# Performance work log

Measured on AMD Instinct MI355X. Metric: run time of the kernel, lower is better.

The kernel has to match this reference:

```python
import jax, jax.numpy as jnp
import numpy as np

# Keras GRUCell (reset_after=True, default in TF2) step
# Keras LSTMCell step (gate order i, f, c, o)
# Keras RNN masking semantics: at masked steps, states are frozen and the
# step output is the previous output (equivalent to freezing every layer's h).

def _gru_step(a, h, W, U, bi, br):
    gx = a @ W + bi          # [B, 3H] input projection
    gh = h @ U + br          # [B, 3H] recurrent projection (reset_after)
    xz, xr, xh = jnp.split(gx, 3, axis=-1)
    rz, rr, rh = jnp.split(gh, 3, axis=-1)
    z = jax.nn.sigmoid(xz + rz)
    r = jax.nn.sigmoid(xr + rr)
    hh = jnp.tanh(xh + r * rh)
    return z * h + (1.0 - z) * hh


def _lstm_step(a, h, c, W, U, b):
    g = a @ W + h @ U + b    # [B, 4H]
    gi, gf, gc, go = jnp.split(g, 4, axis=-1)
    i = jax.nn.sigmoid(gi)
    f = jax.nn.sigmoid(gf)
    cn = f * c + i * jnp.tanh(gc)
    hn = jax.nn.sigmoid(go) * jnp.tanh(cn)
    return hn, cn


def run_gru_stack(x, mask, layers):
    # x: [B,T,D], mask: [B,T] bool; layers: list of (W,U,bi,br)
    B = x.shape[0]
    H = layers[0][1].shape[0]
    xT = jnp.swapaxes(x, 0, 1)      # [T,B,D]
    mT = jnp.swapaxes(mask, 0, 1)   # [T,B]

    def step(hs, inp):
        xt, mt = inp
        a = xt
        new = []
        for (W, U, bi, br), h in zip(layers, hs):
            hn = _gru_step(a, h, W, U, bi, br)
            hn = jnp.where(mt[:, None], hn, h)  # freeze state under mask
            new.append(hn)
            a = hn
        return tuple(new), a

    h0 = tuple(jnp.zeros((B, H), x.dtype) for _ in layers)
    _, ys = jax.lax.scan(step, h0, (xT, mT))
    return jnp.swapaxes(ys, 0, 1)   # [B,T,H]


def run_lstm_stack(x, mask, layers):
    # layers: list of (W,U,b)
    B = x.shape[0]
    H = layers[0][1].shape[0]
    xT = jnp.swapaxes(x, 0, 1)
    mT = jnp.swapaxes(mask, 0, 1)

    def step(state, inp):
        xt, mt = inp
        a = xt
        new = []
        for (W, U, b), (h, c) in zip(layers, state):
            hn, cn = _lstm_step(a, h, c, W, U, b)
            hn = jnp.where(mt[:, None], hn, h)
            cn = jnp.where(mt[:, None], cn, c)
            new.append((hn, cn))
            a = hn
        return tuple(new), a

    s0 = tuple((jnp.zeros((B, H), x.dtype), jnp.zeros((B, H), x.dtype)) for _ in layers)
    _, ys = jax.lax.scan(step, s0, (xT, mT))
    return jnp.swapaxes(ys, 0, 1)


def _forward(x, lengths, g_W0, g_U0, g_bi0, g_br0, g_W1, g_U1, g_bi1, g_br1,
             l_W0, l_U0, l_b0, l_W1, l_U1, l_b1, out_W, out_b):
    T = x.shape[1]
    mask = jnp.arange(T)[None, :] < lengths[:, None]          # [B,T]
    o1 = run_gru_stack(x, mask, [(g_W0, g_U0, g_bi0, g_br0),
                                 (g_W1, g_U1, g_bi1, g_br1)])  # [B,T,H]
    o2 = run_lstm_stack(x, mask, [(l_W0, l_U0, l_b0),
                                  (l_W1, l_U1, l_b1)])          # [B,T,H]
    c = jnp.concatenate([o1, o2], axis=-1)                      # [B,T,2H]
    return c @ out_W + out_b                                    # [B,T,1]


def setup_inputs() -> dict:
    key = jax.random.key(0)
    ks = jax.random.split(key, 16)
    B, T, D, H = 64, 512, 96, 256
    glorot = lambda k, shp: (jax.random.normal(k, shp, dtype=jnp.float32)
                             / np.sqrt(shp[0]).astype(np.float32))
    inp = {
        "x": jax.random.normal(ks[0], (B, T, D), dtype=jnp.float32),
        "lengths": jax.random.randint(ks[1], (B,), 1, T + 1),
        # GRU stack (reset_after: separate input/recurrent biases)
        "g_W0": glorot(ks[2], (D, 3 * H)),
        "g_U0": glorot(ks[3], (H, 3 * H)),
        "g_bi0": jnp.zeros((3 * H,), jnp.float32),
        "g_br0": jnp.zeros((3 * H,), jnp.float32),
        "g_W1": glorot(ks[4], (H, 3 * H)),
        "g_U1": glorot(ks[5], (H, 3 * H)),
        "g_bi1": jnp.zeros((3 * H,), jnp.float32),
        "g_br1": jnp.zeros((3 * H,), jnp.float32),
        # LSTM stack
        "l_W0": glorot(ks[6], (D, 4 * H)),
        "l_U0": glorot(ks[7], (H, 4 * H)),
        "l_b0": jnp.zeros((4 * H,), jnp.float32),
        "l_W1": glorot(ks[8], (H, 4 * H)),
        "l_U1": glorot(ks[9], (H, 4 * H)),
        "l_b1": jnp.zeros((4 * H,), jnp.float32),
        # Dense head on concat [.., 2H] -> 1
        "out_W": glorot(ks[10], (2 * H, 1)),
        "out_b": jnp.zeros((1,), jnp.float32),
    }
    return inp


def reference(x, lengths, g_W0, g_U0, g_bi0, g_br0, g_W1, g_U1, g_bi1, g_br1,
              l_W0, l_U0, l_b0, l_W1, l_U1, l_b1, out_W, out_b):
    return _forward(x, lengths, g_W0, g_U0, g_bi0, g_br0, g_W1, g_U1, g_bi1,
                    g_br1, l_W0, l_U0, l_b0, l_W1, l_U1, l_b1, out_W, out_b)
```

## Files before the change

kernel.cpp:

```cpp
#include <hip/hip_runtime.h>
#include <hip/hip_fp16.h>

constexpr int Tt = 512, Dd = 96, Hh = 256;
constexpr int NS0 = 16;
constexpr int NSP = 8;
typedef unsigned long long u64;

constexpr size_t OFF_P0  = (size_t)4 << 20;
constexpr size_t OFF_P1  = (size_t)12 << 20;
constexpr size_t OFF_FLG = (size_t)20 << 20;
constexpr size_t OFF_W16 = ((size_t)20 << 20) + ((size_t)64 << 10);
constexpr size_t oGW0 = 0;
constexpr size_t oGU0 = oGW0 + (size_t)48 * 768;
constexpr size_t oGW1 = oGU0 + (size_t)128 * 768;
constexpr size_t oGU1 = oGW1 + (size_t)128 * 768;
constexpr size_t oLW0 = oGU1 + (size_t)128 * 768;
constexpr size_t oLU0 = oLW0 + (size_t)48 * 1024;
constexpr size_t oLW1 = oLU0 + (size_t)128 * 1024;
constexpr size_t oLU1 = oLW1 + (size_t)128 * 1024;

__device__ __forceinline__ float sigf(float v) { return 1.0f / (1.0f + __expf(-v)); }
__device__ __forceinline__ u64 agld(const u64* p) {
    return __hip_atomic_load(p, __ATOMIC_RELAXED, __HIP_MEMORY_SCOPE_AGENT);
}
__device__ __forceinline__ int agldi(const int* p) {
    return __hip_atomic_load(p, __ATOMIC_ACQUIRE, __HIP_MEMORY_SCOPE_AGENT);
}
__device__ __forceinline__ void agst(u64* p, u64 v) {
    __hip_atomic_store(p, v, __ATOMIC_RELAXED, __HIP_MEMORY_SCOPE_AGENT);
}

__device__ __forceinline__ float dot2f(unsigned w, unsigned a, float acc) {
#if __has_builtin(__builtin_amdgcn_fdot2)
    typedef _Float16 h2v __attribute__((ext_vector_type(2)));
    h2v wh, ah;
    __builtin_memcpy(&wh, &w, 4);
    __builtin_memcpy(&ah, &a, 4);
    return __builtin_amdgcn_fdot2(wh, ah, acc, false);
#else
    const float2 wf = __half22float2(*(const __half2*)&w);
    const float2 af = __half22float2(*(const __half2*)&a);
    acc = fmaf(wf.x, af.x, acc);
    return fmaf(wf.y, af.y, acc);
#endif
}

__device__ __forceinline__ int hidx(int k, int r) {
    return (k >> 1) * 8 + r * 2 + (k & 1);
}

template<int G>
__device__ __forceinline__ void load4h(uint4* wv, const uint4* __restrict__ M4,
                                       int ldm, int kpb) {
    const int base = (kpb >> 2) * ldm;
    #pragma unroll
    for (int g = 0; g < G; ++g)
        wv[g] = M4[base + g * 256];
}
template<int G>
__device__ __forceinline__ void fma4h(const uint4* wv, const uint4* __restrict__ A4,
                                      int kpb, float4* acc) {
    const uint4 a0 = A4[kpb + 0];
    const uint4 a1 = A4[kpb + 1];
    const uint4 a2 = A4[kpb + 2];
    const uint4 a3 = A4[kpb + 3];
    #pragma unroll
    for (int g = 0; g < G; ++g) {
        const uint4 w = wv[g];
        acc[g].x = dot2f(w.x, a0.x, acc[g].x);
        acc[g].y = dot2f(w.x, a0.y, acc[g].y);
        acc[g].z = dot2f(w.x, a0.z, acc[g].z);
        acc[g].w = dot2f(w.x, a0.w, acc[g].w);
        acc[g].x = dot2f(w.y, a1.x, acc[g].x);
        acc[g].y = dot2f(w.y, a1.y, acc[g].y);
        acc[g].z = dot2f(w.y, a1.z, acc[g].z);
        acc[g].w = dot2f(w.y, a1.w, acc[g].w);
        acc[g].x = dot2f(w.z, a2.x, acc[g].x);
        acc[g].y = dot2f(w.z, a2.y, acc[g].y);
        acc[g].z = dot2f(w.z, a2.z, acc[g].z);
        acc[g].w = dot2f(w.z, a2.w, acc[g].w);
        acc[g].x = dot2f(w.w, a3.x, acc[g].x);
        acc[g].y = dot2f(w.w, a3.y, acc[g].y);
        acc[g].z = dot2f(w.w, a3.z, acc[g].z);
        acc[g].w = dot2f(w.w, a3.w, acc[g].w);
    }
}
template<int G>
__device__ __forceinline__ void gemmP(const uint4* __restrict__ M4, int ldm,
                                      const uint4* __restrict__ A4,
                                      int kp0, int kp1, float4* acc) {
    const int n4 = (kp1 - kp0) >> 2;
    uint4 wv0[G], wv1[G];
    if (n4 <= 0) return;
    load4h<G>(wv0, M4, ldm, kp0);
    int c2 = 0;
    for (; c2 + 2 <= n4; c2 += 2) {
        load4h<G>(wv1, M4, ldm, kp0 + (c2 + 1) * 4);
        fma4h<G>(wv0, A4, kp0 + c2 * 4, acc);
        if (c2 + 2 < n4) load4h<G>(wv0, M4, ldm, kp0 + (c2 + 2) * 4);
        fma4h<G>(wv1, A4, kp0 + (c2 + 1) * 4, acc);
    }
    if (c2 < n4) fma4h<G>(wv0, A4, kp0 + c2 * 4, acc);
}

__global__ void cvt_pair(const float* __restrict__ src, unsigned* __restrict__ dst,
                         int n, int ld) {
    const int i = blockIdx.x * 256 + threadIdx.x;
    if (i >= n) return;
    const int kp = i / ld, col = i - kp * ld;
    const __half2 h = __floats2half2_rn(src[(2 * kp) * ld + col],
                                        src[(2 * kp + 1) * ld + col]);
    dst[((size_t)((kp >> 2) * ld + col) << 2) + (kp & 3)] = *(const unsigned*)&h;
}

__global__ void __launch_bounds__(1024, 4)
rnn_persist(const float* __restrict__ x, const int* __restrict__ lengths,
            const float* __restrict__ gbi0, const float* __restrict__ gbr0,
            const float* __restrict__ gbi1, const float* __restrict__ gbr1,
            const float* __restrict__ lb0, const float* __restrict__ lb1,
            const float* __restrict__ outW, const float* __restrict__ outb,
            float* __restrict__ out, char* __restrict__ wsb)
{
    const int tid = threadIdx.x;
    const int c   = tid & 255;
    const int grp = tid >> 8;
    const int bx  = blockIdx.x;
    const int role  = bx & 3;
    const int chain = (bx >> 2) & 1;
    const int rg    = bx >> 3;
    const int rowbase = rg * 4;

    const int GA  = chain ? 4 : 3;
    const int GAH = GA * Hh;

    u64* h0ring = (u64*)wsb + (size_t)(chain * 16 + rg) * (NS0 * 1024);
    u64* p0ring = (u64*)(wsb + OFF_P0) + (size_t)(chain * 16 + rg) * (NSP * 4096);
    u64* p1ring = (u64*)(wsb + OFF_P1) + (size_t)(chain * 16 + rg) * (NSP * 4096);
    int* flags = (int*)(wsb + OFF_FLG);
    int* flg_r0 = flags + ((chain * 16 + rg) * 4 + 1) * 32;
    int* flg_p1 = flags + ((chain * 16 + rg) * 4 + 2) * 32;
    int* flg_r1 = flags + ((chain * 16 + rg) * 4 + 3) * 32;

    const unsigned* W16 = (const unsigned*)(wsb + OFF_W16);
    size_t woff;
    if (chain == 0) woff = (role == 0) ? oGW0 : (role == 1) ? oGU0 : (role == 2) ? oGW1 : oGU1;
    else            woff = (role == 0) ? oLW0 : (role == 1) ? oLU0 : (role == 2) ? oLW1 : oLU1;
    const uint4* M4 = (const uint4*)(W16 + woff) + c;

    const int KR  = (role == 0) ? Dd : Hh;
    const int KP2 = KR >> 3;
    const int kp0 = grp * KP2, kp1 = kp0 + KP2;

    __shared__ __align__(16) unsigned sAh[128 * 4];
    __shared__ float sG[2 * 4096];
    __shared__ float sP[4096];
    __shared__ float sRed[16];
    __half* sAhh = (__half*)sAh;
    const uint4* A4 = (const uint4*)sAh;

    const int NP  = 4 * GAH;
    const int npt = NP >> 10;
    float biasv[4];
    int sgidx[4];
    if (role == 0 || role == 2) {
        const float* bsrc = (chain == 0) ? (role == 0 ? gbi0 : gbi1)
                                         : (role == 0 ? lb0 : lb1);
        #pragma unroll
        for (int i = 0; i < 4; ++i) {
            if (i < npt) {
                const int e = tid + i * 1024;
                const int r = e / GAH, rem = e - r * GAH;
                biasv[i] = bsrc[rem];
                sgidx[i] = r * 1024 + rem;
            } else { biasv[i] = 0; sgidx[i] = 0; }
        }
    }
    const int rA = grp;
    const int lenA = lengths[rowbase + rA];
    float brz = 0, brr = 0, brh = 0, ow = 0;
    if (chain == 0 && (role == 1 || role == 3)) {
        const float* br = (role == 1) ? gbr0 : gbr1;
        brz = br[c]; brr = br[Hh + c]; brh = br[2 * Hh + c];
    }
    if (role == 3) ow = outW[chain * Hh + c];
    const float outb0 = outb[0];
    float creg = 0.0f;
    float hprev = 0.0f;

    for (int i = tid; i < 512; i += 1024) sAh[i] = 0;
    __syncthreads();

    for (int t = 0; t < Tt; ++t) {
        if (role == 0) {
            if (t >= NSP) {
                if (tid == 0)
                    while (agldi(flg_r0) < t - NSP + 1) __builtin_amdgcn_s_sleep(1);
                __syncthreads();
            }
            if (tid < 4 * Dd) {
                const int r = tid / Dd, k = tid - r * Dd;
                const float v = x[((size_t)(rowbase + r) * Tt + t) * Dd + k];
                sAhh[hidx(k, r)] = __float2half(v);
            }
            __syncthreads();
        } else if (role == 2) {
            const u64* p0 = h0ring + (size_t)(t & (NS0 - 1)) * 1024 + rA * 256 + c;
            const unsigned want = (unsigned)(t + 1);
            u64 v0;
            do { v0 = agld(p0); } while ((unsigned)v0 != want);
            sAhh[hidx(c, rA)] = __float2half(__uint_as_float((unsigned)(v0 >> 32)));
            __syncthreads();
            if (tid == 0)
                __hip_atomic_exchange(flg_p1, t + 1, __ATOMIC_RELEASE,
                                      __HIP_MEMORY_SCOPE_AGENT);
        } else {
            const u64* slot = ((role == 1) ? p0ring : p1ring)
                              + (size_t)(t & (NSP - 1)) * 4096;
            const unsigned want = (unsigned)(t + 1);
            unsigned dm = 0;
            const unsigned full = (1u << npt) - 1u;
            while (dm != full) {
                for (int i = 0; i < npt; ++i) {
                    if (!(dm & (1u << i))) {
                        const u64 v = agld(slot + tid + i * 1024);
                        if ((unsigned)v == want) {
                            sP[tid + i * 1024] = __uint_as_float((unsigned)(v >> 32));
                            dm |= 1u << i;
                        }
                    }
                }
            }
            __syncthreads();
            if (tid == 0)
                __hip_atomic_exchange((role == 1) ? flg_r0 : flg_r1, t + 1,
                                      __ATOMIC_RELEASE, __HIP_MEMORY_SCOPE_AGENT);
        }

        if (chain == 0) {
            float4 acc[3] = {{0,0,0,0},{0,0,0,0},{0,0,0,0}};
            gemmP<3>(M4, GAH, A4, kp0, kp1, acc);
            if (grp < 2) {
                #pragma unroll
                for (int g = 0; g < 3; ++g) {
                    sG[grp * 4096 + 0 + g * 256 + c]    = acc[g].x;
                    sG[grp * 4096 + 1024 + g * 256 + c] = acc[g].y;
                    sG[grp * 4096 + 2048 + g * 256 + c] = acc[g].z;
                    sG[grp * 4096 + 3072 + g * 256 + c] = acc[g].w;
                }
            }
            __syncthreads();
            if (grp >= 2) {
                const int b = (grp - 2) * 4096;
                #pragma unroll
                for (int g = 0; g < 3; ++g) {
                    sG[b + 0 + g * 256 + c]    += acc[g].x;
                    sG[b + 1024 + g * 256 + c] += acc[g].y;
                    sG[b + 2048 + g * 256 + c] += acc[g].z;
                    sG[b + 3072 + g * 256 + c] += acc[g].w;
                }
            }
        } else {
            float4 acc[4] = {{0,0,0,0},{0,0,0,0},{0,0,0,0},{0,0,0,0}};
            gemmP<4>(M4, GAH, A4, kp0, kp1, acc);
            if (grp < 2) {
                #pragma unroll
                for (int g = 0; g < 4; ++g) {
                    sG[grp * 4096 + 0 + g * 256 + c]    = acc[g].x;
                    sG[grp * 4096 + 1024 + g * 256 + c] = acc[g].y;
                    sG[grp * 4096 + 2048 + g * 256 + c] = acc[g].z;
                    sG[grp * 4096 + 3072 + g * 256 + c] = acc[g].w;
                }
            }
            __syncthreads();
            if (grp >= 2) {
                const int b = (grp - 2) * 4096;
                #pragma unroll
                for (int g = 0; g < 4; ++g) {
                    sG[b + 0 + g * 256 + c]    += acc[g].x;
                    sG[b + 1024 + g * 256 + c] += acc[g].y;
                    sG[b + 2048 + g * 256 + c] += acc[g].z;
                    sG[b + 3072 + g * 256 + c] += acc[g].w;
                }
            }
        }
        __syncthreads();

        if (role == 0 || role == 2) {
            if (role == 2 && t >= NSP) {
                if (tid == 0)
                    while (agldi(flg_r1) < t - NSP + 1) __builtin_amdgcn_s_sleep(1);
                __syncthreads();
            }
            u64* ring = (role == 0) ? p0ring : p1ring;
            u64* slot = ring + (size_t)(t & (NSP - 1)) * 4096;
            for (int i = 0; i < npt; ++i) {
                const float v = sG[sgidx[i]] + sG[4096 + sgidx[i]] + biasv[i];
                agst(slot + tid + i * 1024,
                     ((u64)__float_as_uint(v) << 32) | (unsigned)(t + 1));
            }
        } else {
            if (role == 1 && t >= NS0) {
                if (tid == 0)
                    while (agldi(flg_p1) < t - NS0 + 1) __builtin_amdgcn_s_sleep(1);
                __syncthreads();
            }
            const int r = rA;
            const float hold = hprev;
            float hn;
            if (chain == 0) {
                const float Pz = sP[r * GAH + c];
                const float Pr = sP[r * GAH + Hh + c];
                const float Ph = sP[r * GAH + 2 * Hh + c];
                const float Qz = sG[r * 1024 + c]       + sG[4096 + r * 1024 + c];
                const float Qr = sG[r * 1024 + 256 + c] + sG[4096 + r * 1024 + 256 + c];
                const float Qh = sG[r * 1024 + 512 + c] + sG[4096 + r * 1024 + 512 + c];
                const float z  = sigf(Pz + Qz + brz);
                const float rr = sigf(Pr + Qr + brr);
                const float hh = tanhf(Ph + rr * (Qh + brh));
                hn = z * hold + (1.0f - z) * hh;
                if (t >= lenA) hn = hold;
            } else {
                const float gi = sP[r * GAH + c]          + sG[r * 1024 + c]       + sG[4096 + r * 1024 + c];
                const float gf = sP[r * GAH + Hh + c]     + sG[r * 1024 + 256 + c] + sG[4096 + r * 1024 + 256 + c];
                const float gc = sP[r * GAH + 2 * Hh + c] + sG[r * 1024 + 512 + c] + sG[4096 + r * 1024 + 512 + c];
                const float go = sP[r * GAH + 3 * Hh + c] + sG[r * 1024 + 768 + c] + sG[4096 + r * 1024 + 768 + c];
                float cn = sigf(gf) * creg + sigf(gi) * tanhf(gc);
                hn = sigf(go) * tanhf(cn);
                if (t >= lenA) { hn = hold; cn = creg; }
                creg = cn;
            }
            hprev = hn;
            sAhh[hidx(c, r)] = __float2half(hn);
            if (role == 1) {
                agst(h0ring + (size_t)(t & (NS0 - 1)) * 1024 + r * 256 + c,
                     ((u64)__float_as_uint(hn) << 32) | (unsigned)(t + 1));
            } else {
                float vh = hn * ow;
                for (int o = 32; o > 0; o >>= 1)
                    vh += __shfl_down(vh, o);
                if ((tid & 63) == 0) sRed[tid >> 6] = vh;
                __syncthreads();
                if (tid < 4) {
                    const float s = sRed[tid * 4] + sRed[tid * 4 + 1]
                                  + sRed[tid * 4 + 2] + sRed[tid * 4 + 3];
                    atomicAdd(&out[(size_t)(rowbase + tid) * Tt + t],
                              s + (chain ? outb0 : 0.0f));
                }
            }
        }
        __syncthreads();
    }
}

extern "C" void kernel_launch(void* const* d_in, const int* in_sizes, int n_in,
                              void* d_out, int out_size, void* d_ws, size_t ws_size,
                              hipStream_t stream) {
    const float* x       = (const float*)d_in[0];
    const int*   lengths = (const int*)d_in[1];
    const float* gW0  = (const float*)d_in[2];
    const float* gU0  = (const float*)d_in[3];
    const float* gbi0 = (const float*)d_in[4];
    const float* gbr0 = (const float*)d_in[5];
    const float* gW1  = (const float*)d_in[6];
    const float* gU1  = (const float*)d_in[7];
    const float* gbi1 = (const float*)d_in[8];
    const float* gbr1 = (const float*)d_in[9];
    const float* lW0  = (const float*)d_in[10];
    const float* lU0  = (const float*)d_in[11];
    const float* lb0  = (const float*)d_in[12];
    const float* lW1  = (const float*)d_in[13];
    const float* lU1  = (const float*)d_in[14];
    const float* lb1  = (const float*)d_in[15];
    const float* outW = (const float*)d_in[16];
    const float* outb = (const float*)d_in[17];
    float* out = (float*)d_out;
    char* wsb  = (char*)d_ws;

    hipMemsetAsync(d_ws, 0, OFF_FLG + (16 << 10), stream);
    hipMemsetAsync(d_out, 0, (size_t)out_size * sizeof(float), stream);

    unsigned* W16 = (unsigned*)(wsb + OFF_W16);
    struct { const float* s; size_t o; int K; int ld; } cv[8] = {
        {gW0, oGW0, 96, 768}, {gU0, oGU0, 256, 768},
        {gW1, oGW1, 256, 768}, {gU1, oGU1, 256, 768},
        {lW0, oLW0, 96, 1024}, {lU0, oLU0, 256, 1024},
        {lW1, oLW1, 256, 1024}, {lU1, oLU1, 256, 1024},
    };
    for (int i = 0; i < 8; ++i) {
        const int n = (cv[i].K / 2) * cv[i].ld;
        cvt_pair<<<(n + 255) / 256, 256, 0, stream>>>(cv[i].s, W16 + cv[i].o, n, cv[i].ld);
    }

    rnn_persist<<<dim3(128), dim3(1024), 0, stream>>>(
        x, lengths, gbi0, gbr0, gbi1, gbr1, lb0, lb1, outW, outb, out, wsb);
}
```

Baseline: 5.410 ms.

## Split RNN persistent kernel into 8 roles per chain with column-sliced weights

Restructures the persistent RNN kernel from 4 roles of 1024 threads to 8 roles of 512 threads per chain/row-group (256 blocks). Each layer's recurrent matmul is now split across two or four blocks by hidden-unit slices, and each recurrent block computes its own gate nonlinearity. Layer-1 blocks fuse the W1/U1 products instead of going through a separate projection ring. Weights are reconverted into per-slice fp16 layouts, and synchronisation now uses multiple per-slice flags plus a new h1 ring. The aim is to shorten the per-timestep critical path by spreading the recurrent GEMV over more CUs, at the cost of more cross-block polling traffic and sync points.

```diff
diff --git a/kernel.cpp b/kernel.cpp
--- a/kernel.cpp
+++ b/kernel.cpp
@@ -3,21 +3,22 @@
 
 constexpr int Tt = 512, Dd = 96, Hh = 256;
 constexpr int NS0 = 16;
+constexpr int NS1 = 16;
 constexpr int NSP = 8;
 typedef unsigned long long u64;
 
+constexpr size_t OFF_H0  = 0;
 constexpr size_t OFF_P0  = (size_t)4 << 20;
-constexpr size_t OFF_P1  = (size_t)12 << 20;
+constexpr size_t OFF_H1  = (size_t)12 << 20;
 constexpr size_t OFF_FLG = (size_t)20 << 20;
 constexpr size_t OFF_W16 = ((size_t)20 << 20) + ((size_t)64 << 10);
-constexpr size_t oGW0 = 0;
-constexpr size_t oGU0 = oGW0 + (size_t)48 * 768;
-constexpr size_t oGW1 = oGU0 + (size_t)128 * 768;
-constexpr size_t oGU1 = oGW1 + (size_t)128 * 768;
-constexpr size_t oLW0 = oGU1 + (size_t)128 * 768;
-constexpr size_t oLU0 = oLW0 + (size_t)48 * 1024;
-constexpr size_t oLW1 = oLU0 + (size_t)128 * 1024;
-constexpr size_t oLU1 = oLW1 + (size_t)128 * 1024;
+
+constexpr size_t sG_p0 = (size_t)384 * 48,  oG_p0 = 0;
+constexpr size_t sG_r0 = (size_t)384 * 128, oG_r0 = oG_p0 + 2 * sG_p0;
+constexpr size_t sG_r1 = (size_t)192 * 256, oG_r1 = oG_r0 + 2 * sG_r0;
+constexpr size_t sL_p0 = (size_t)512 * 48,  oL_p0 = oG_r1 + 4 * sG_r1;
+constexpr size_t sL_r0 = (size_t)512 * 128, oL_r0 = oL_p0 + 2 * sL_p0;
+constexpr size_t sL_r1 = (size_t)256 * 256, oL_r1 = oL_r0 + 2 * sL_r0;
 
 __device__ __forceinline__ float sigf(float v) { return 1.0f / (1.0f + __expf(-v)); }
 __device__ __forceinline__ u64 agld(const u64* p) {
@@ -28,6 +29,22 @@
 }
 __device__ __forceinline__ void agst(u64* p, u64 v) {
     __hip_atomic_store(p, v, __ATOMIC_RELAXED, __HIP_MEMORY_SCOPE_AGENT);
+}
+__device__ __forceinline__ void xrel(int* p, int v) {
+    __hip_atomic_exchange(p, v, __ATOMIC_RELEASE, __HIP_MEMORY_SCOPE_AGENT);
+}
+__device__ __forceinline__ float pollF(const u64* p, unsigned want) {
+    u64 v = agld(p);
+    while ((unsigned)v != want) v = agld(p);
+    return __uint_as_float((unsigned)(v >> 32));
+}
+__device__ __forceinline__ void waitFlags(const int* flg, int fid0, int n, int need) {
+    for (;;) {
+        int m = 0x7fffffff;
+        for (int i = 0; i < n; ++i) m = min(m, agldi(flg + (fid0 + i) * 32));
+        if (m >= need) break;
+        __builtin_amdgcn_s_sleep(1);
+    }
 }
 
 __device__ __forceinline__ float dot2f(unsigned w, unsigned a, float acc) {
@@ -49,71 +66,71 @@
     return (k >> 1) * 8 + r * 2 + (k & 1);
 }
 
-template<int G>
-__device__ __forceinline__ void load4h(uint4* wv, const uint4* __restrict__ M4,
-                                       int ldm, int kpb) {
-    const int base = (kpb >> 2) * ldm;
-    #pragma unroll
-    for (int g = 0; g < G; ++g)
-        wv[g] = M4[base + g * 256];
-}
-template<int G>
-__device__ __forceinline__ void fma4h(const uint4* wv, const uint4* __restrict__ A4,
-                                      int kpb, float4* acc) {
-    const uint4 a0 = A4[kpb + 0];
-    const uint4 a1 = A4[kpb + 1];
-    const uint4 a2 = A4[kpb + 2];
-    const uint4 a3 = A4[kpb + 3];
-    #pragma unroll
-    for (int g = 0; g < G; ++g) {
-        const uint4 w = wv[g];
-        acc[g].x = dot2f(w.x, a0.x, acc[g].x);
-        acc[g].y = dot2f(w.x, a0.y, acc[g].y);
-        acc[g].z = dot2f(w.x, a0.z, acc[g].z);
-        acc[g].w = dot2f(w.x, a0.w, acc[g].w);
-        acc[g].x = dot2f(w.y, a1.x, acc[g].x);
-        acc[g].y = dot2f(w.y, a1.y, acc[g].y);
-        acc[g].z = dot2f(w.y, a1.z, acc[g].z);
-        acc[g].w = dot2f(w.y, a1.w, acc[g].w);
-        acc[g].x = dot2f(w.z, a2.x, acc[g].x);
-        acc[g].y = dot2f(w.z, a2.y, acc[g].y);
-        acc[g].z = dot2f(w.z, a2.z, acc[g].z);
-        acc[g].w = dot2f(w.z, a2.w, acc[g].w);
-        acc[g].x = dot2f(w.w, a3.x, acc[g].x);
-        acc[g].y = dot2f(w.w, a3.y, acc[g].y);
-        acc[g].z = dot2f(w.w, a3.z, acc[g].z);
-        acc[g].w = dot2f(w.w, a3.w, acc[g].w);
-    }
-}
-template<int G>
-__device__ __forceinline__ void gemmP(const uint4* __restrict__ M4, int ldm,
-                                      const uint4* __restrict__ A4,
-                                      int kp0, int kp1, float4* acc) {
-    const int n4 = (kp1 - kp0) >> 2;
-    uint4 wv0[G], wv1[G];
-    if (n4 <= 0) return;
-    load4h<G>(wv0, M4, ldm, kp0);
-    int c2 = 0;
-    for (; c2 + 2 <= n4; c2 += 2) {
-        load4h<G>(wv1, M4, ldm, kp0 + (c2 + 1) * 4);
-        fma4h<G>(wv0, A4, kp0 + c2 * 4, acc);
-        if (c2 + 2 < n4) load4h<G>(wv0, M4, ldm, kp0 + (c2 + 2) * 4);
-        fma4h<G>(wv1, A4, kp0 + (c2 + 1) * 4, acc);
-    }
-    if (c2 < n4) fma4h<G>(wv0, A4, kp0 + c2 * 4, acc);
-}
-
-__global__ void cvt_pair(const float* __restrict__ src, unsigned* __restrict__ dst,
-                         int n, int ld) {
+__device__ __forceinline__ void fmaC(const uint4 w, const uint4* __restrict__ A4,
+                                     int kpb, float4& a) {
+    const uint4 a0 = A4[kpb + 0], a1 = A4[kpb + 1], a2 = A4[kpb + 2], a3 = A4[kpb + 3];
+    a.x = dot2f(w.x, a0.x, a.x); a.y = dot2f(w.x, a0.y, a.y);
+    a.z = dot2f(w.x, a0.z, a.z); a.w = dot2f(w.x, a0.w, a.w);
+    a.x = dot2f(w.y, a1.x, a.x); a.y = dot2f(w.y, a1.y, a.y);
+    a.z = dot2f(w.y, a1.z, a.z); a.w = dot2f(w.y, a1.w, a.w);
+    a.x = dot2f(w.z, a2.x, a.x); a.y = dot2f(w.z, a2.y, a.y);
+    a.z = dot2f(w.z, a2.z, a.z); a.w = dot2f(w.z, a2.w, a.w);
+    a.x = dot2f(w.w, a3.x, a.x); a.y = dot2f(w.w, a3.y, a.y);
+    a.z = dot2f(w.w, a3.z, a.z); a.w = dot2f(w.w, a3.w, a.w);
+}
+
+__device__ __forceinline__ void gemmG2(const uint4* __restrict__ Mc, int NC,
+                                       const uint4* __restrict__ A4,
+                                       int kp0, int n4, float4& X0, float4& X1) {
+    int cb = kp0 >> 2;
+    uint4 p0 = Mc[(size_t)cb * NC], p1 = Mc[(size_t)cb * NC + 256];
+    for (int i = 0; i < n4; ++i) {
+        uint4 q0 = p0, q1 = p1;
+        if (i + 1 < n4) {
+            q0 = Mc[(size_t)(cb + 1) * NC];
+            q1 = Mc[(size_t)(cb + 1) * NC + 256];
+        }
+        fmaC(p0, A4, cb * 4, X0);
+        fmaC(p1, A4, cb * 4, X1);
+        p0 = q0; p1 = q1; ++cb;
+    }
+}
+
+__device__ __forceinline__ void gemmG1(const uint4* __restrict__ Mc, int NC,
+                                       const uint4* __restrict__ A4,
+                                       int kp0, int n4, float4& X0) {
+    int cb = kp0 >> 2;
+    uint4 w0 = Mc[(size_t)(cb + 0) * NC], w1 = Mc[(size_t)(cb + 1) * NC],
+          w2 = Mc[(size_t)(cb + 2) * NC], w3 = Mc[(size_t)(cb + 3) * NC];
+    for (int i = 0; i < n4; i += 4) {
+        uint4 n0 = w0, n1 = w1, n2 = w2, n3 = w3;
+        if (i + 4 < n4) {
+            n0 = Mc[(size_t)(cb + 4) * NC]; n1 = Mc[(size_t)(cb + 5) * NC];
+            n2 = Mc[(size_t)(cb + 6) * NC]; n3 = Mc[(size_t)(cb + 7) * NC];
+        }
+        fmaC(w0, A4, (cb + 0) * 4, X0);
+        fmaC(w1, A4, (cb + 1) * 4, X0);
+        fmaC(w2, A4, (cb + 2) * 4, X0);
+        fmaC(w3, A4, (cb + 3) * 4, X0);
+        w0 = n0; w1 = n1; w2 = n2; w3 = n3; cb += 4;
+    }
+}
+
+__global__ void cvt_slice(const float* __restrict__ src, unsigned* __restrict__ dst,
+                          int srcN, int kpTot, int NC, int NUs, int u0, int kOff) {
     const int i = blockIdx.x * 256 + threadIdx.x;
-    if (i >= n) return;
-    const int kp = i / ld, col = i - kp * ld;
-    const __half2 h = __floats2half2_rn(src[(2 * kp) * ld + col],
-                                        src[(2 * kp + 1) * ld + col]);
-    dst[((size_t)((kp >> 2) * ld + col) << 2) + (kp & 3)] = *(const unsigned*)&h;
-}
-
-__global__ void __launch_bounds__(1024, 4)
+    const int total = kpTot * NC;
+    if (i >= total) return;
+    const int kp = i / NC, j = i - kp * NC;
+    const int g = j >> NUs, u = j & ((1 << NUs) - 1);
+    const int scol = g * 256 + u0 + u;
+    const __half2 h = __floats2half2_rn(src[(size_t)(2 * kp) * srcN + scol],
+                                        src[(size_t)(2 * kp + 1) * srcN + scol]);
+    const int dkp = kp + kOff;
+    dst[((size_t)(dkp >> 2) * NC + j) * 4 + (dkp & 3)] = *(const unsigned*)&h;
+}
+
+__global__ void __launch_bounds__(512, 1)
 rnn_persist(const float* __restrict__ x, const int* __restrict__ lengths,
             const float* __restrict__ gbi0, const float* __restrict__ gbr0,
             const float* __restrict__ gbi1, const float* __restrict__ gbr1,
@@ -125,230 +142,242 @@
     const int c   = tid & 255;
     const int grp = tid >> 8;
     const int bx  = blockIdx.x;
-    const int role  = bx & 3;
-    const int chain = (bx >> 2) & 1;
-    const int rg    = bx >> 3;
+    const int role  = bx & 7;
+    const int chain = (bx >> 3) & 1;
+    const int rg    = bx >> 4;
     const int rowbase = rg * 4;
-
-    const int GA  = chain ? 4 : 3;
-    const int GAH = GA * Hh;
-
-    u64* h0ring = (u64*)wsb + (size_t)(chain * 16 + rg) * (NS0 * 1024);
-    u64* p0ring = (u64*)(wsb + OFF_P0) + (size_t)(chain * 16 + rg) * (NSP * 4096);
-    u64* p1ring = (u64*)(wsb + OFF_P1) + (size_t)(chain * 16 + rg) * (NSP * 4096);
-    int* flags = (int*)(wsb + OFF_FLG);
-    int* flg_r0 = flags + ((chain * 16 + rg) * 4 + 1) * 32;
-    int* flg_p1 = flags + ((chain * 16 + rg) * 4 + 2) * 32;
-    int* flg_r1 = flags + ((chain * 16 + rg) * 4 + 3) * 32;
+    const int kind = (role < 2) ? 0 : (role < 4) ? 1 : 2;
+    const int sub  = (kind == 0) ? role : (kind == 1) ? role - 2 : role - 4;
+
+    const int NG  = chain ? 4 : 3;
+    const int GAH = NG * 256;
+
+    const int grpid = chain * 16 + rg;
+    u64* h0ring = (u64*)(wsb + OFF_H0) + (size_t)grpid * (NS0 * 1024);
+    u64* p0ring = (u64*)(wsb + OFF_P0) + (size_t)grpid * (NSP * 4096);
+    u64* h1ring = (u64*)(wsb + OFF_H1) + (size_t)grpid * (NS1 * 1024);
+    int* flg    = (int*)(wsb + OFF_FLG) + grpid * (16 * 32);
 
     const unsigned* W16 = (const unsigned*)(wsb + OFF_W16);
-    size_t woff;
-    if (chain == 0) woff = (role == 0) ? oGW0 : (role == 1) ? oGU0 : (role == 2) ? oGW1 : oGU1;
-    else            woff = (role == 0) ? oLW0 : (role == 1) ? oLU0 : (role == 2) ? oLW1 : oLU1;
-    const uint4* M4 = (const uint4*)(W16 + woff) + c;
-
-    const int KR  = (role == 0) ? Dd : Hh;
-    const int KP2 = KR >> 3;
-    const int kp0 = grp * KP2, kp1 = kp0 + KP2;
-
-    __shared__ __align__(16) unsigned sAh[128 * 4];
-    __shared__ float sG[2 * 4096];
-    __shared__ float sP[4096];
-    __shared__ float sRed[16];
+    size_t woff; int NC, KPh;
+    if (chain == 0) {
+        if (kind == 0)      { woff = oG_p0 + (size_t)sub * sG_p0; NC = 384; KPh = 24; }
+        else if (kind == 1) { woff = oG_r0 + (size_t)sub * sG_r0; NC = 384; KPh = 64; }
+        else                { woff = oG_r1 + (size_t)sub * sG_r1; NC = 192; KPh = 128; }
+    } else {
+        if (kind == 0)      { woff = oL_p0 + (size_t)sub * sL_p0; NC = 512; KPh = 24; }
+        else if (kind == 1) { woff = oL_r0 + (size_t)sub * sL_r0; NC = 512; KPh = 64; }
+        else                { woff = oL_r1 + (size_t)sub * sL_r1; NC = 256; KPh = 128; }
+    }
+    const uint4* Mc = (const uint4*)(W16 + woff) + c;
+    const int kp0 = grp * KPh;
+    const int n4  = KPh >> 2;
+
+    __shared__ __align__(16) unsigned sAh[1024];
+    __shared__ float sG[8 * 512];
     __half* sAhh = (__half*)sAh;
     const uint4* A4 = (const uint4*)sAh;
 
-    const int NP  = 4 * GAH;
-    const int npt = NP >> 10;
-    float biasv[4];
-    int sgidx[4];
-    if (role == 0 || role == 2) {
-        const float* bsrc = (chain == 0) ? (role == 0 ? gbi0 : gbi1)
-                                         : (role == 0 ? lb0 : lb1);
+    const int u0 = sub * 128;
+    const int q0 = sub * 64;
+
+    int ringoff[4]; int sgi[4]; float biasv[4];
+    if (kind == 0) {
+        const float* bsrc = chain ? lb0 : gbi0;
         #pragma unroll
         for (int i = 0; i < 4; ++i) {
-            if (i < npt) {
-                const int e = tid + i * 1024;
-                const int r = e / GAH, rem = e - r * GAH;
-                biasv[i] = bsrc[rem];
-                sgidx[i] = r * 1024 + rem;
-            } else { biasv[i] = 0; sgidx[i] = 0; }
-        }
-    }
-    const int rA = grp;
-    const int lenA = lengths[rowbase + rA];
-    float brz = 0, brr = 0, brh = 0, ow = 0;
-    if (chain == 0 && (role == 1 || role == 3)) {
-        const float* br = (role == 1) ? gbr0 : gbr1;
-        brz = br[c]; brr = br[Hh + c]; brh = br[2 * Hh + c];
-    }
-    if (role == 3) ow = outW[chain * Hh + c];
+            if (i < NG) {
+                const int e = tid + i * 512;
+                const int r = e / NC, j = e - r * NC;
+                const int g = j >> 7, uL = j & 127;
+                ringoff[i] = r * GAH + g * 256 + u0 + uL;
+                biasv[i]   = bsrc[g * 256 + u0 + uL];
+                sgi[i]     = r * 512 + j;
+            } else { ringoff[i] = 0; biasv[i] = 0.0f; sgi[i] = 0; }
+        }
+    }
+    const int rr1 = tid >> 7, uu1 = tid & 127;
+    const int rr2 = (tid >> 6) & 3, uu2 = tid & 63;
+    float br_[4] = {0, 0, 0, 0};
+    if (kind == 1 && chain == 0)
+        for (int g = 0; g < 3; ++g) br_[g] = gbr0[g * 256 + u0 + uu1];
+    float biW[4] = {0, 0, 0, 0}, brU[4] = {0, 0, 0, 0}, ow = 0.0f;
+    if (kind == 2 && tid < 256) {
+        if (chain == 0) {
+            for (int g = 0; g < 3; ++g) {
+                biW[g] = gbi1[g * 256 + q0 + uu2];
+                brU[g] = gbr1[g * 256 + q0 + uu2];
+            }
+        } else {
+            for (int g = 0; g < 4; ++g) biW[g] = lb1[g * 256 + q0 + uu2];
+        }
+        ow = outW[chain * Hh + q0 + uu2];
+    }
+    int lenR = Tt + 1;
+    if (kind == 1) lenR = lengths[rowbase + rr1];
+    if (kind == 2 && tid < 256) lenR = lengths[rowbase + rr2];
     const float outb0 = outb[0];
-    float creg = 0.0f;
-    float hprev = 0.0f;
-
-    for (int i = tid; i < 512; i += 1024) sAh[i] = 0;
+    float hprev = 0.0f, creg = 0.0f;
+
+    for (int i = tid; i < 1024; i += 512) sAh[i] = 0;
     __syncthreads();
 
     for (int t = 0; t < Tt; ++t) {
-        if (role == 0) {
+        if (kind == 0) {
             if (t >= NSP) {
-                if (tid == 0)
-                    while (agldi(flg_r0) < t - NSP + 1) __builtin_amdgcn_s_sleep(1);
+                if (tid == 0) waitFlags(flg, sub, 1, t - NSP + 1);
                 __syncthreads();
             }
             if (tid < 4 * Dd) {
                 const int r = tid / Dd, k = tid - r * Dd;
-                const float v = x[((size_t)(rowbase + r) * Tt + t) * Dd + k];
-                sAhh[hidx(k, r)] = __float2half(v);
-            }
-            __syncthreads();
-        } else if (role == 2) {
-            const u64* p0 = h0ring + (size_t)(t & (NS0 - 1)) * 1024 + rA * 256 + c;
-            const unsigned want = (unsigned)(t + 1);
-            u64 v0;
-            do { v0 = agld(p0); } while ((unsigned)v0 != want);
-            sAhh[hidx(c, rA)] = __float2half(__uint_as_float((unsigned)(v0 >> 32)));
-            __syncthreads();
-            if (tid == 0)
-                __hip_atomic_exchange(flg_p1, t + 1, __ATOMIC_RELEASE,
-                                      __HIP_MEMORY_SCOPE_AGENT);
+                sAhh[hidx(k, r)] =
+                    __float2half(x[((size_t)(rowbase + r) * Tt + t) * Dd + k]);
+            }
+        } else if (kind == 1) {
+            if (t > 0) {
+                const u64* base = h0ring + (size_t)((t - 1) & (NS0 - 1)) * 1024;
+                const int pu0 = 128 - u0;
+                const float v = pollF(base + rr1 * 256 + pu0 + uu1, (unsigned)t);
+                sAhh[hidx(pu0 + uu1, rr1)] = __float2half(v);
+            }
         } else {
-            const u64* slot = ((role == 1) ? p0ring : p1ring)
-                              + (size_t)(t & (NSP - 1)) * 4096;
-            const unsigned want = (unsigned)(t + 1);
-            unsigned dm = 0;
-            const unsigned full = (1u << npt) - 1u;
-            while (dm != full) {
-                for (int i = 0; i < npt; ++i) {
-                    if (!(dm & (1u << i))) {
-                        const u64 v = agld(slot + tid + i * 1024);
-                        if ((unsigned)v == want) {
-                            sP[tid + i * 1024] = __uint_as_float((unsigned)(v >> 32));
-                            dm |= 1u << i;
-                        }
-                    }
+            const u64* b0 = h0ring + (size_t)(t & (NS0 - 1)) * 1024;
+            #pragma unroll
+            for (int i = 0; i < 2; ++i) {
+                const int e = tid + i * 512, un = e & 255, r = e >> 8;
+                sAhh[hidx(un, r)] =
+                    __float2half(pollF(b0 + r * 256 + un, (unsigned)(t + 1)));
+            }
+            if (t > 0) {
+                const u64* b1 = h1ring + (size_t)((t - 1) & (NS1 - 1)) * 1024;
+                #pragma unroll
+                for (int i = 0; i < 2; ++i) {
+                    const int e = tid + i * 512, un = e & 255, r = e >> 8;
+                    sAhh[hidx(256 + un, r)] =
+                        __float2half(pollF(b1 + r * 256 + un, (unsigned)t));
                 }
             }
-            __syncthreads();
-            if (tid == 0)
-                __hip_atomic_exchange((role == 1) ? flg_r0 : flg_r1, t + 1,
-                                      __ATOMIC_RELEASE, __HIP_MEMORY_SCOPE_AGENT);
-        }
-
-        if (chain == 0) {
-            float4 acc[3] = {{0,0,0,0},{0,0,0,0},{0,0,0,0}};
-            gemmP<3>(M4, GAH, A4, kp0, kp1, acc);
-            if (grp < 2) {
-                #pragma unroll
-                for (int g = 0; g < 3; ++g) {
-                    sG[grp * 4096 + 0 + g * 256 + c]    = acc[g].x;
-                    sG[grp * 4096 + 1024 + g * 256 + c] = acc[g].y;
-                    sG[grp * 4096 + 2048 + g * 256 + c] = acc[g].z;
-                    sG[grp * 4096 + 3072 + g * 256 + c] = acc[g].w;
+        }
+        __syncthreads();
+
+        if (kind <= 1) {
+            float4 X0 = {0, 0, 0, 0}, X1 = {0, 0, 0, 0};
+            gemmG2(Mc, NC, A4, kp0, n4, X0, X1);
+            const int b = grp * 2048;
+            sG[b + 0 * 512 + c] = X0.x; sG[b + 1 * 512 + c] = X0.y;
+            sG[b + 2 * 512 + c] = X0.z; sG[b + 3 * 512 + c] = X0.w;
+            if (c + 256 < NC) {
+                sG[b + 0 * 512 + 256 + c] = X1.x; sG[b + 1 * 512 + 256 + c] = X1.y;
+                sG[b + 2 * 512 + 256 + c] = X1.z; sG[b + 3 * 512 + 256 + c] = X1.w;
+            }
+        } else {
+            float4 X0 = {0, 0, 0, 0};
+            gemmG1(Mc, NC, A4, kp0, n4, X0);
+            const int b = grp * 2048;
+            sG[b + 0 * 512 + c] = X0.x; sG[b + 1 * 512 + c] = X0.y;
+            sG[b + 2 * 512 + c] = X0.z; sG[b + 3 * 512 + c] = X0.w;
+        }
+        __syncthreads();
+
+        if (kind == 0) {
+            u64* slot = p0ring + (size_t)(t & (NSP - 1)) * 4096;
+            #pragma unroll
+            for (int i = 0; i < 4; ++i) {
+                if (i < NG) {
+                    const float v = sG[sgi[i]] + sG[2048 + sgi[i]] + biasv[i];
+                    agst(slot + ringoff[i],
+                         ((u64)__float_as_uint(v) << 32) | (unsigned)(t + 1));
                 }
             }
-            __syncthreads();
-            if (grp >= 2) {
-                const int b = (grp - 2) * 4096;
-                #pragma unroll
-                for (int g = 0; g < 3; ++g) {
-                    sG[b + 0 + g * 256 + c]    += acc[g].x;
-                    sG[b + 1024 + g * 256 + c] += acc[g].y;
-                    sG[b + 2048 + g * 256 + c] += acc[g].z;
-                    sG[b + 3072 + g * 256 + c] += acc[g].w;
+        } else if (kind == 1) {
+            const u64* pslot = p0ring + (size_t)(t & (NSP - 1)) * 4096;
+            float P[4] = {0, 0, 0, 0}, Q[4] = {0, 0, 0, 0};
+            #pragma unroll
+            for (int g = 0; g < 4; ++g) {
+                if (g < NG) {
+                    P[g] = pollF(pslot + rr1 * GAH + g * 256 + u0 + uu1,
+                                 (unsigned)(t + 1));
+                    const int j = g * 128 + uu1;
+                    Q[g] = sG[rr1 * 512 + j] + sG[2048 + rr1 * 512 + j];
                 }
             }
-        } else {
-            float4 acc[4] = {{0,0,0,0},{0,0,0,0},{0,0,0,0},{0,0,0,0}};
-            gemmP<4>(M4, GAH, A4, kp0, kp1, acc);
-            if (grp < 2) {
-                #pragma unroll
-                for (int g = 0; g < 4; ++g) {
-                    sG[grp * 4096 + 0 + g * 256 + c]    = acc[g].x;
-                    sG[grp * 4096 + 1024 + g * 256 + c] = acc[g].y;
-                    sG[grp * 4096 + 2048 + g * 256 + c] = acc[g].z;
-                    sG[grp * 4096 + 3072 + g * 256 + c] = acc[g].w;
-                }
-            }
-            __syncthreads();
-            if (grp >= 2) {
-                const int b = (grp - 2) * 4096;
-                #pragma unroll
-                for (int g = 0; g < 4; ++g) {
-                    sG[b + 0 + g * 256 + c]    += acc[g].x;
-                    sG[b + 1024 + g * 256 + c] += acc[g].y;
-                    sG[b + 2048 + g * 256 + c] += acc[g].z;
-                    sG[b + 3072 + g * 256 + c] += acc[g].w;
-                }
-            }
-        }
-        __syncthreads();
-
-        if (role == 0 || role == 2) {
-            if (role == 2 && t >= NSP) {
-                if (tid == 0)
-                    while (agldi(flg_r1) < t - NSP + 1) __builtin_amdgcn_s_sleep(1);
-                __syncthreads();
-            }
-            u64* ring = (role == 0) ? p0ring : p1ring;
-            u64* slot = ring + (size_t)(t & (NSP - 1)) * 4096;
-            for (int i = 0; i < npt; ++i) {
-                const float v = sG[sgidx[i]] + sG[4096 + sgidx[i]] + biasv[i];
-                agst(slot + tid + i * 1024,
-                     ((u64)__float_as_uint(v) << 32) | (unsigned)(t + 1));
-            }
-        } else {
-            if (role == 1 && t >= NS0) {
-                if (tid == 0)
-                    while (agldi(flg_p1) < t - NS0 + 1) __builtin_amdgcn_s_sleep(1);
-                __syncthreads();
-            }
-            const int r = rA;
             const float hold = hprev;
             float hn;
             if (chain == 0) {
-                const float Pz = sP[r * GAH + c];
-                const float Pr = sP[r * GAH + Hh + c];
-                const float Ph = sP[r * GAH + 2 * Hh + c];
-                const float Qz = sG[r * 1024 + c]       + sG[4096 + r * 1024 + c];
-                const float Qr = sG[r * 1024 + 256 + c] + sG[4096 + r * 1024 + 256 + c];
-                const float Qh = sG[r * 1024 + 512 + c] + sG[4096 + r * 1024 + 512 + c];
-                const float z  = sigf(Pz + Qz + brz);
-                const float rr = sigf(Pr + Qr + brr);
-                const float hh = tanhf(Ph + rr * (Qh + brh));
+                const float z  = sigf(P[0] + Q[0] + br_[0]);
+                const float r_ = sigf(P[1] + Q[1] + br_[1]);
+                const float hh = tanhf(P[2] + r_ * (Q[2] + br_[2]));
                 hn = z * hold + (1.0f - z) * hh;
-                if (t >= lenA) hn = hold;
+                if (t >= lenR) hn = hold;
             } else {
-                const float gi = sP[r * GAH + c]          + sG[r * 1024 + c]       + sG[4096 + r * 1024 + c];
-                const float gf = sP[r * GAH + Hh + c]     + sG[r * 1024 + 256 + c] + sG[4096 + r * 1024 + 256 + c];
-                const float gc = sP[r * GAH + 2 * Hh + c] + sG[r * 1024 + 512 + c] + sG[4096 + r * 1024 + 512 + c];
-                const float go = sP[r * GAH + 3 * Hh + c] + sG[r * 1024 + 768 + c] + sG[4096 + r * 1024 + 768 + c];
-                float cn = sigf(gf) * creg + sigf(gi) * tanhf(gc);
-                hn = sigf(go) * tanhf(cn);
-                if (t >= lenA) { hn = hold; cn = creg; }
+                float cn = sigf(P[1] + Q[1]) * creg
+                         + sigf(P[0] + Q[0]) * tanhf(P[2] + Q[2]);
+                hn = sigf(P[3] + Q[3]) * tanhf(cn);
+                if (t >= lenR) { hn = hold; cn = creg; }
                 creg = cn;
             }
             hprev = hn;
-            sAhh[hidx(c, r)] = __float2half(hn);
-            if (role == 1) {
-                agst(h0ring + (size_t)(t & (NS0 - 1)) * 1024 + r * 256 + c,
+            if (t >= NS0) {
+                if (tid == 0) waitFlags(flg, 2, 6, t - NS0 + 1);
+                __syncthreads();
+            }
+            agst(h0ring + (size_t)(t & (NS0 - 1)) * 1024 + rr1 * 256 + u0 + uu1,
+                 ((u64)__float_as_uint(hn) << 32) | (unsigned)(t + 1));
+            sAhh[hidx(u0 + uu1, rr1)] = __float2half(hn);
+        } else {
+            const bool act = tid < 256;
+            float hn = 0.0f;
+            if (act) {
+                float W[4] = {0, 0, 0, 0}, U[4] = {0, 0, 0, 0};
+                #pragma unroll
+                for (int g = 0; g < 4; ++g) {
+                    if (g < NG) {
+                        const int j = g * 64 + uu2;
+                        W[g] = sG[rr2 * 512 + j] + biW[g];
+                        U[g] = sG[2048 + rr2 * 512 + j] + brU[g];
+                    }
+                }
+                const float hold = hprev;
+                if (chain == 0) {
+                    const float z  = sigf(W[0] + U[0]);
+                    const float r_ = sigf(W[1] + U[1]);
+                    const float hh = tanhf(W[2] + r_ * U[2]);
+                    hn = z * hold + (1.0f - z) * hh;
+                    if (t >= lenR) hn = hold;
+                } else {
+                    float cn = sigf(W[1] + U[1]) * creg
+                             + sigf(W[0] + U[0]) * tanhf(W[2] + U[2]);
+                    hn = sigf(W[3] + U[3]) * tanhf(cn);
+                    if (t >= lenR) { hn = hold; cn = creg; }
+                    creg = cn;
+                }
+                hprev = hn;
+            }
+            if (t >= NS1) {
+                if (tid == 0) waitFlags(flg, 8, 4, t - NS1 + 1);
+                __syncthreads();
+            }
+            if (act) {
+                agst(h1ring + (size_t)(t & (NS1 - 1)) * 1024 + rr2 * 256 + q0 + uu2,
                      ((u64)__float_as_uint(hn) << 32) | (unsigned)(t + 1));
-            } else {
                 float vh = hn * ow;
-                for (int o = 32; o > 0; o >>= 1)
-                    vh += __shfl_down(vh, o);
-                if ((tid & 63) == 0) sRed[tid >> 6] = vh;
-                __syncthreads();
-                if (tid < 4) {
-                    const float s = sRed[tid * 4] + sRed[tid * 4 + 1]
-                                  + sRed[tid * 4 + 2] + sRed[tid * 4 + 3];
-                    atomicAdd(&out[(size_t)(rowbase + tid) * Tt + t],
-                              s + (chain ? outb0 : 0.0f));
-                }
+                #pragma unroll
+                for (int o = 32; o > 0; o >>= 1) vh += __shfl_down(vh, o);
+                if ((tid & 63) == 0)
+                    atomicAdd(&out[(size_t)(rowbase + rr2) * Tt + t],
+                              vh + ((chain == 1 && sub == 0) ? outb0 : 0.0f));
             }
         }
         __syncthreads();
+        if (tid == 0) {
+            if (kind == 1) {
+                xrel(flg + (0 + sub) * 32, t + 1);
+                xrel(flg + (2 + sub) * 32, t);
+            } else if (kind == 2) {
+                xrel(flg + (4 + sub) * 32, t + 1);
+                xrel(flg + (8 + sub) * 32, t);
+            }
+        }
     }
 }
 
@@ -376,21 +405,35 @@
     float* out = (float*)d_out;
     char* wsb  = (char*)d_ws;
 
-    hipMemsetAsync(d_ws, 0, OFF_FLG + (16 << 10), stream);
+    hipMemsetAsync(d_ws, 0, OFF_W16, stream);
     hipMemsetAsync(d_out, 0, (size_t)out_size * sizeof(float), stream);
 
     unsigned* W16 = (unsigned*)(wsb + OFF_W16);
-    struct { const float* s; size_t o; int K; int ld; } cv[8] = {
-        {gW0, oGW0, 96, 768}, {gU0, oGU0, 256, 768},
-        {gW1, oGW1, 256, 768}, {gU1, oGU1, 256, 768},
-        {lW0, oLW0, 96, 1024}, {lU0, oLU0, 256, 1024},
-        {lW1, oLW1, 256, 1024}, {lU1, oLU1, 256, 1024},
-    };
-    for (int i = 0; i < 8; ++i) {
-        const int n = (cv[i].K / 2) * cv[i].ld;
-        cvt_pair<<<(n + 255) / 256, 256, 0, stream>>>(cv[i].s, W16 + cv[i].o, n, cv[i].ld);
-    }
-
-    rnn_persist<<<dim3(128), dim3(1024), 0, stream>>>(
+    struct CV { const float* s; size_t off; int srcN, kpTot, NC, NUs, u0, kOff; };
+    CV cv[24]; int n = 0;
+    for (int sub = 0; sub < 2; ++sub)
+        cv[n++] = {gW0, oG_p0 + sub * sG_p0, 768, 48, 384, 7, sub * 128, 0};
+    for (int sub = 0; sub < 2; ++sub)
+        cv[n++] = {gU0, oG_r0 + sub * sG_r0, 768, 128, 384, 7, sub * 128, 0};
+    for (int sub = 0; sub < 4; ++sub) {
+        cv[n++] = {gW1, oG_r1 + sub * sG_r1, 768, 128, 192, 6, sub * 64, 0};
+        cv[n++] = {gU1, oG_r1 + sub * sG_r1, 768, 128, 192, 6, sub * 64, 128};
+    }
+    for (int sub = 0; sub < 2; ++sub)
+        cv[n++] = {lW0, oL_p0 + sub * sL_p0, 1024, 48, 512, 7, sub * 128, 0};
+    for (int sub = 0; sub < 2; ++sub)
+        cv[n++] = {lU0, oL_r0 + sub * sL_r0, 1024, 128, 512, 7, sub * 128, 0};
+    for (int sub = 0; sub < 4; ++sub) {
+        cv[n++] = {lW1, oL_r1 + sub * sL_r1, 1024, 128, 256, 6, sub * 64, 0};
+        cv[n++] = {lU1, oL_r1 + sub * sL_r1, 1024, 128, 256, 6, sub * 64, 128};
+    }
+    for (int i = 0; i < 24; ++i) {
+        const int tot = cv[i].kpTot * cv[i].NC;
+        cvt_slice<<<(tot + 255) / 256, 256, 0, stream>>>(
+            cv[i].s, W16 + cv[i].off, cv[i].srcN, cv[i].kpTot, cv[i].NC,
+            cv[i].NUs, cv[i].u0, cv[i].kOff);
+    }
+
+    rnn_persist<<<dim3(256), dim3(512), 0, stream>>>(
         x, lengths, gbi0, gbr0, gbi1, gbr1, lb0, lb1, outW, outb, out, wsb);
 }
```

Result: slower. 10.83 ms (+100.2%).

## Defer input-projection ring polling until after recurrent GEMM in recurrent roles

Applied to the files above, without the earlier changes.

Recurrent-role blocks no longer wait for the producer's projected-input slot before running their recurrent GEMM. Each thread now polls only its own gate values straight into registers after the GEMM, which drops the shared sP staging buffer and a barrier. The ring-release flag moves to the end of the step. This overlaps the cross-block wait with the recurrent matmul on the critical path, at the cost of the producer's slot being released later.

```diff
diff --git a/kernel.cpp b/kernel.cpp
--- a/kernel.cpp
+++ b/kernel.cpp
@@ -153,7 +153,6 @@
 
     __shared__ __align__(16) unsigned sAh[128 * 4];
     __shared__ float sG[2 * 4096];
-    __shared__ float sP[4096];
     __shared__ float sRed[16];
     __half* sAhh = (__half*)sAh;
     const uint4* A4 = (const uint4*)sAh;
@@ -213,27 +212,6 @@
             if (tid == 0)
                 __hip_atomic_exchange(flg_p1, t + 1, __ATOMIC_RELEASE,
                                       __HIP_MEMORY_SCOPE_AGENT);
-        } else {
-            const u64* slot = ((role == 1) ? p0ring : p1ring)
-                              + (size_t)(t & (NSP - 1)) * 4096;
-            const unsigned want = (unsigned)(t + 1);
-            unsigned dm = 0;
-            const unsigned full = (1u << npt) - 1u;
-            while (dm != full) {
-                for (int i = 0; i < npt; ++i) {
-                    if (!(dm & (1u << i))) {
-                        const u64 v = agld(slot + tid + i * 1024);
-                        if ((unsigned)v == want) {
-                            sP[tid + i * 1024] = __uint_as_float((unsigned)(v >> 32));
-                            dm |= 1u << i;
-                        }
-                    }
-                }
-            }
-            __syncthreads();
-            if (tid == 0)
-                __hip_atomic_exchange((role == 1) ? flg_r0 : flg_r1, t + 1,
-                                      __ATOMIC_RELEASE, __HIP_MEMORY_SCOPE_AGENT);
         }
 
         if (chain == 0) {
@@ -299,6 +277,24 @@
                      ((u64)__float_as_uint(v) << 32) | (unsigned)(t + 1));
             }
         } else {
+            const u64* slot = ((role == 1) ? p0ring : p1ring)
+                              + (size_t)(t & (NSP - 1)) * 4096 + rA * GAH + c;
+            const unsigned want = (unsigned)(t + 1);
+            float P_[4] = {0, 0, 0, 0};
+            unsigned dm = 0;
+            const unsigned full = (1u << GA) - 1u;
+            while (dm != full) {
+                #pragma unroll
+                for (int g = 0; g < 4; ++g) {
+                    if (g < GA && !(dm & (1u << g))) {
+                        const u64 v = agld(slot + g * 256);
+                        if ((unsigned)v == want) {
+                            P_[g] = __uint_as_float((unsigned)(v >> 32));
+                            dm |= 1u << g;
+                        }
+                    }
+                }
+            }
             if (role == 1 && t >= NS0) {
                 if (tid == 0)
                     while (agldi(flg_p1) < t - NS0 + 1) __builtin_amdgcn_s_sleep(1);
@@ -308,22 +304,19 @@
             const float hold = hprev;
             float hn;
             if (chain == 0) {
-                const float Pz = sP[r * GAH + c];
-                const float Pr = sP[r * GAH + Hh + c];
-                const float Ph = sP[r * GAH + 2 * Hh + c];
                 const float Qz = sG[r * 1024 + c]       + sG[4096 + r * 1024 + c];
                 const float Qr = sG[r * 1024 + 256 + c] + sG[4096 + r * 1024 + 256 + c];
                 const float Qh = sG[r * 1024 + 512 + c] + sG[4096 + r * 1024 + 512 + c];
-                const float z  = sigf(Pz + Qz + brz);
-                const float rr = sigf(Pr + Qr + brr);
-                const float hh = tanhf(Ph + rr * (Qh + brh));
+                const float z  = sigf(P_[0] + Qz + brz);
+                const float rr = sigf(P_[1] + Qr + brr);
+                const float hh = tanhf(P_[2] + rr * (Qh + brh));
                 hn = z * hold + (1.0f - z) * hh;
                 if (t >= lenA) hn = hold;
             } else {
-                const float gi = sP[r * GAH + c]          + sG[r * 1024 + c]       + sG[4096 + r * 1024 + c];
-                const float gf = sP[r * GAH + Hh + c]     + sG[r * 1024 + 256 + c] + sG[4096 + r * 1024 + 256 + c];
-                const float gc = sP[r * GAH + 2 * Hh + c] + sG[r * 1024 + 512 + c] + sG[4096 + r * 1024 + 512 + c];
-                const float go = sP[r * GAH + 3 * Hh + c] + sG[r * 1024 + 768 + c] + sG[4096 + r * 1024 + 768 + c];
+                const float gi = P_[0] + sG[r * 1024 + c]       + sG[4096 + r * 1024 + c];
+                const float gf = P_[1] + sG[r * 1024 + 256 + c] + sG[4096 + r * 1024 + 256 + c];
+                const float gc = P_[2] + sG[r * 1024 + 512 + c] + sG[4096 + r * 1024 + 512 + c];
+                const float go = P_[3] + sG[r * 1024 + 768 + c] + sG[4096 + r * 1024 + 768 + c];
                 float cn = sigf(gf) * creg + sigf(gi) * tanhf(gc);
                 hn = sigf(go) * tanhf(cn);
                 if (t >= lenA) { hn = hold; cn = creg; }
@@ -349,6 +342,10 @@
             }
         }
         __syncthreads();
+        if (tid == 0 && (role == 1 || role == 3)) {
+            __hip_atomic_exchange((role == 1) ? flg_r0 : flg_r1, t + 1,
+                                  __ATOMIC_RELEASE, __HIP_MEMORY_SCOPE_AGENT);
+        }
     }
 }
 
```

Measured after the change: 4.890 ms. -9.6%, faster.
